# Performance work log

Measured on AMD Instinct MI355X. Metric: run time of the kernel, lower is better.

## Reference

```python
import jax, jax.numpy as jnp
import numpy as np

E = 1024   # embedding_dim
H = 16     # num_head
D = 64     # dim_head (E == H*D)
R = 8      # LoRA rank
BATCH = 2
SEQ = 2048
EPS = 1e-6


def setup_inputs() -> dict:
    key = jax.random.key(0)
    ks = jax.random.split(key, 16)
    s = 0.02
    return {
        "y": jax.random.normal(ks[0], (BATCH, SEQ, E), jnp.float32),
        "Wqkv": jax.random.normal(ks[1], (3 * E, E), jnp.float32) * s,
        "bqkv": jax.random.normal(ks[2], (3 * E,), jnp.float32) * s,
        "Wmsa": jax.random.normal(ks[3], (E, E), jnp.float32) * s,
        "Bq": jax.random.normal(ks[4], (E, R), jnp.float32) * s,
        "Aq": jax.random.normal(ks[5], (R, E), jnp.float32) * s,
        "Bk": jax.random.normal(ks[6], (E, R), jnp.float32) * s,
        "Ak": jax.random.normal(ks[7], (R, E), jnp.float32) * s,
        "Bv": jax.random.normal(ks[8], (E, R), jnp.float32) * s,
        "Av": jax.random.normal(ks[9], (R, E), jnp.float32) * s,
        "Bo": jax.random.normal(ks[10], (E, R), jnp.float32) * s,
        "Ao": jax.random.normal(ks[11], (R, E), jnp.float32) * s,
        "gamma": jnp.ones((E,), jnp.float32),
        "beta": jnp.zeros((E,), jnp.float32),
        "i": 0,
    }


def reference(y, Wqkv, bqkv, Wmsa, Bq, Aq, Bk, Ak, Bv, Av, Bo, Ao, gamma, beta, i):
    B, S, En = y.shape
    # fused QKV projection: nn.Linear -> y @ W.T + b
    qkv = (y @ Wqkv.T + bqkv).reshape(B, S, 3, H, D).transpose(2, 0, 3, 1, 4)
    Q, K, V = qkv[0], qkv[1], qkv[2]          # each [B,H,S,D]

    def lora_delta(Bw, Aw):
        # torch: y @ (B.weight @ A.weight), reshaped to heads
        return (y @ (Bw @ Aw)).reshape(B, S, H, D).transpose(0, 2, 1, 3)

    Q = Q + lora_delta(Bq, Aq)
    K = K + lora_delta(Bk, Ak)
    V = V + lora_delta(Bv, Av)

    scale = jnp.asarray(np.sqrt(D), y.dtype)
    scores = jnp.einsum('bhqd,bhkd->bhqk', Q, K) / scale
    attn = jax.nn.softmax(scores, axis=-1)
    o = jnp.einsum('bhqk,bhkd->bhqd', attn, V)          # [B,H,S,D]
    o = o.transpose(0, 2, 1, 3).reshape(B, S, H * D)    # [B,S,E]

    msa = o @ Wmsa.T + o @ (Bo @ Ao)
    res = msa + y

    mu = jnp.mean(res, axis=-1, keepdims=True)
    var = jnp.var(res, axis=-1, keepdims=True)
    return (res - mu) * jax.lax.rsqrt(var + EPS) * gamma + beta
```

## Files before the change

kernel.cpp:

```cpp
#include <hip/hip_runtime.h>
#include <hip/hip_bf16.h>
#include <stdint.h>

typedef __attribute__((ext_vector_type(8))) short short8;
typedef __attribute__((ext_vector_type(4))) float f32x4;

typedef const __attribute__((address_space(1))) void gv_t;
typedef __attribute__((address_space(3))) void lv_t;

#define SCQ 0.18033688011112042f

__device__ __forceinline__ void gl_lds16(const void* g, void* l) {
    __builtin_amdgcn_global_load_lds((gv_t*)g, (lv_t*)l, 16, 0, 0);
}

__device__ __forceinline__ unsigned short f2bf(float f) {
    union { float f; unsigned int u; } v; v.f = f;
    unsigned int r = v.u + 0x7fffu + ((v.u >> 16) & 1u);
    return (unsigned short)(r >> 16);
}

__device__ __forceinline__ unsigned int pack2bf(float a, float b) {
    union { __hip_bfloat162 h2; unsigned int u; } cv;
    cv.h2 = __float22bfloat162_rn(make_float2(a, b));
    return cv.u;
}

__device__ __forceinline__ f32x4 zero4() { f32x4 z = {0.f, 0.f, 0.f, 0.f}; return z; }

__global__ void k_cvt(const float* __restrict__ y, unsigned short* __restrict__ yb) {
    int i = (blockIdx.x * 256 + threadIdx.x) * 4;
    float4 v = *(const float4*)(y + i);
    union { unsigned short u[4]; uint2 w; } o;
    o.u[0] = f2bf(v.x); o.u[1] = f2bf(v.y); o.u[2] = f2bf(v.z); o.u[3] = f2bf(v.w);
    *(uint2*)(yb + i) = o.w;
}

__global__ void k_wqkv(const float* __restrict__ W,
                       const float* __restrict__ Bq, const float* __restrict__ Aq,
                       const float* __restrict__ Bk, const float* __restrict__ Ak,
                       const float* __restrict__ Bv, const float* __restrict__ Av,
                       unsigned short* __restrict__ out) {
    int idx = blockIdx.x * 256 + threadIdx.x;
    int n = idx >> 10, k = idx & 1023;
    int sel = n >> 10, n0 = n & 1023;
    const float* Bp = (sel == 0) ? Bq : (sel == 1) ? Bk : Bv;
    const float* Ap = (sel == 0) ? Aq : (sel == 1) ? Ak : Av;
    float acc = W[idx];
    #pragma unroll
    for (int r = 0; r < 8; ++r) acc += Bp[k * 8 + r] * Ap[r * 1024 + n0];
    out[idx] = f2bf(acc * ((sel == 0) ? SCQ : 1.0f));
}

__global__ void k_wmsa(const float* __restrict__ W,
                       const float* __restrict__ Bo, const float* __restrict__ Ao,
                       unsigned short* __restrict__ out) {
    int idx = blockIdx.x * 256 + threadIdx.x;
    int n = idx >> 10, k = idx & 1023;
    float acc = W[idx];
    #pragma unroll
    for (int r = 0; r < 8; ++r) acc += Bo[k * 8 + r] * Ao[r * 1024 + n];
    out[idx] = f2bf(acc);
}

template <int TM, int EPI>
__global__ __launch_bounds__(256, 2) void k_gemm(const unsigned short* __restrict__ Ag,
                                                 const unsigned short* __restrict__ Bg,
                                                 const float* __restrict__ bias,
                                                 const float* __restrict__ yres,
                                                 void* __restrict__ Cout,
                                                 int M, int N, int K) {
    constexpr int WAVES_N = 256 / TM;
    constexpr int WN = TM / 2;
    constexpr int NI = WN / 16;
    constexpr int ACALLS = TM / 64;
    __shared__ unsigned short As[2][TM * 32];
    __shared__ unsigned short Bs[2][128 * 32];
    const int flat = threadIdx.x;
    const int m0 = blockIdx.y * TM, n0 = blockIdx.x * 128;
    const int lane = flat & 63, wave = flat >> 6;
    const int l16 = lane & 15, quad = lane >> 4;
    const int wm = (wave / WAVES_N) * 64, wn = (wave % WAVES_N) * WN;

    f32x4 acc[4][NI];
    #pragma unroll
    for (int mi = 0; mi < 4; ++mi)
        #pragma unroll
        for (int ni = 0; ni < NI; ++ni) acc[mi][ni] = zero4();

    const unsigned short* ap = Ag + (size_t)(m0 + (flat >> 2)) * K + (flat & 3) * 8;
    const unsigned short* bp = Bg + (size_t)(n0 + (flat >> 2)) * K + (flat & 3) * 8;
    const size_t rstep = (size_t)64 * K;

    #pragma unroll
    for (int c = 0; c < ACALLS; ++c) gl_lds16(ap + c * rstep, &As[0][c * 2048 + flat * 8]);
    gl_lds16(bp,         &Bs[0][flat * 8]);
    gl_lds16(bp + rstep, &Bs[0][2048 + flat * 8]);
    ap += 32; bp += 32;
    __syncthreads();

    for (int k0 = 0; k0 < K; k0 += 32) {
        const int cur = (k0 >> 5) & 1;
        if (k0 + 32 < K) {
            const int nxt = cur ^ 1;
            #pragma unroll
            for (int c = 0; c < ACALLS; ++c) gl_lds16(ap + c * rstep, &As[nxt][c * 2048 + flat * 8]);
            gl_lds16(bp,         &Bs[nxt][flat * 8]);
            gl_lds16(bp + rstep, &Bs[nxt][2048 + flat * 8]);
            ap += 32; bp += 32;
        }

        short8 af[4], bfr[NI];
        #pragma unroll
        for (int i = 0; i < 4; ++i) af[i] = *(const short8*)&As[cur][(wm + i * 16 + l16) * 32 + quad * 8];
        #pragma unroll
        for (int i = 0; i < NI; ++i) bfr[i] = *(const short8*)&Bs[cur][(wn + i * 16 + l16) * 32 + quad * 8];
        #pragma unroll
        for (int mi = 0; mi < 4; ++mi)
            #pragma unroll
            for (int ni = 0; ni < NI; ++ni)
                acc[mi][ni] = __builtin_amdgcn_mfma_f32_16x16x32_bf16(af[mi], bfr[ni], acc[mi][ni], 0, 0, 0);

        __syncthreads();
    }

    if (EPI == 0) {
        unsigned short* C = (unsigned short*)Cout;
        #pragma unroll
        for (int ni = 0; ni < NI; ++ni) {
            int col = n0 + wn + ni * 16 + l16;
            float bv = bias[col] * ((col < 1024) ? SCQ : 1.0f);
            #pragma unroll
            for (int mi = 0; mi < 4; ++mi) {
                int row = m0 + wm + mi * 16 + quad * 4;
                #pragma unroll
                for (int r = 0; r < 4; ++r)
                    C[(size_t)(row + r) * N + col] = f2bf(acc[mi][ni][r] + bv);
            }
        }
    } else {
        float* C = (float*)Cout;
        #pragma unroll
        for (int ni = 0; ni < NI; ++ni) {
            int col = n0 + wn + ni * 16 + l16;
            #pragma unroll
            for (int mi = 0; mi < 4; ++mi) {
                int row = m0 + wm + mi * 16 + quad * 4;
                #pragma unroll
                for (int r = 0; r < 4; ++r)
                    C[(size_t)(row + r) * N + col] = acc[mi][ni][r] + yres[(size_t)(row + r) * N + col];
            }
        }
    }
}

__global__ __launch_bounds__(256) void k_vt(const unsigned short* __restrict__ qkv,
                                            unsigned short* __restrict__ vtg) {
    __shared__ unsigned short T[64 * 72];
    const int t = threadIdx.x;
    const int k0 = blockIdx.x * 64, h = blockIdx.y, b = blockIdx.z;
    const unsigned short* vbase = qkv + (size_t)(b * 2048) * 3072 + 2048 + h * 64;
    #pragma unroll
    for (int i = 0; i < 2; ++i) {
        int B = i * 256 + t;
        int row = B >> 3, c = B & 7;
        short8 v = *(const short8*)(vbase + (size_t)(k0 + row) * 3072 + c * 8);
        *(short8*)&T[row * 72 + c * 8] = v;
    }
    __syncthreads();
    unsigned short* obase = vtg + ((size_t)((b * 16 + h) * 64)) * 2048 + k0;
    #pragma unroll
    for (int i = 0; i < 2; ++i) {
        int B = i * 256 + t;
        int d = B >> 3, kc = B & 7;
        union { unsigned short u[8]; short8 v; } pk;
        #pragma unroll
        for (int jj = 0; jj < 8; ++jj) pk.u[jj] = T[(kc * 8 + jj) * 72 + d];
        *(short8*)(obase + (size_t)d * 2048 + kc * 8) = pk.v;
    }
}

__global__ __launch_bounds__(256, 2) void k_attn(const unsigned short* __restrict__ qkv,
                                                 const unsigned short* __restrict__ vtg,
                                                 unsigned short* __restrict__ o) {
    __shared__ unsigned short LDS[24576];
    unsigned short* Qs = LDS;
    unsigned short* Ps = LDS;
    unsigned short* Ks0 = LDS + 8192;
    unsigned short* Vt0 = LDS + 16384;

    const int t = threadIdx.x;
    const int lane = t & 63, wave = t >> 6;
    const int l16 = lane & 15, quad = lane >> 4;
    const int l8 = l16 & 7;
    const int q0 = blockIdx.x * 128;
    const int h = blockIdx.y, b = blockIdx.z;

    const unsigned short* qbase = qkv + (size_t)(b * 2048) * 3072 + h * 64;
    const unsigned short* kbase = qbase + 1024;
    const unsigned short* vtbase = vtg + (size_t)((b * 16 + h) * 64) * 2048;

    #pragma unroll
    for (int i = 0; i < 4; ++i) {
        int B = i * 256 + t;
        int row = B >> 3, c = (B & 7) ^ (row & 7);
        gl_lds16(qbase + (size_t)(q0 + row) * 3072 + c * 8, &Qs[B * 8]);
    }

    const int B0 = t, B1 = t + 256;
    const int r0 = B0 >> 3, c0 = (B0 & 7) ^ (r0 & 7);
    const int r1 = B1 >> 3, c1 = (B1 & 7) ^ (r1 & 7);
    const unsigned short* kp0 = kbase + (size_t)r0 * 3072 + c0 * 8;
    const unsigned short* kp1 = kbase + (size_t)r1 * 3072 + c1 * 8;
    const unsigned short* vp0 = vtbase + (size_t)r0 * 2048 + c0 * 8;
    const unsigned short* vp1 = vtbase + (size_t)r1 * 2048 + c1 * 8;

    gl_lds16(kp0, &Ks0[B0 * 8]);
    gl_lds16(kp1, &Ks0[B1 * 8]);
    gl_lds16(vp0, &Vt0[B0 * 8]);
    gl_lds16(vp1, &Vt0[B1 * 8]);
    kp0 += 64 * 3072; kp1 += 64 * 3072; vp0 += 64; vp1 += 64;

    __syncthreads();

    short8 qf[2][2];
    #pragma unroll
    for (int ni = 0; ni < 2; ++ni)
        #pragma unroll
        for (int kk = 0; kk < 2; ++kk)
            qf[ni][kk] = *(const short8*)&Qs[(wave * 32 + ni * 16 + l16) * 64 + ((kk * 4 + quad) ^ l8) * 8];

    __syncthreads();

    f32x4 acc_o[2][4];
    #pragma unroll
    for (int mo = 0; mo < 2; ++mo)
        #pragma unroll
        for (int nd = 0; nd < 4; ++nd) acc_o[mo][nd] = zero4();
    float lsum[2] = {0.f, 0.f};

    for (int j = 0; j < 32; ++j) {
        const unsigned short* Ks = Ks0 + (j & 1) * 4096;
        const unsigned short* Vt = Vt0 + (j & 1) * 4096;

        if (j < 31) {
            unsigned short* Kn = Ks0 + ((j + 1) & 1) * 4096;
            unsigned short* Vn = Vt0 + ((j + 1) & 1) * 4096;
            gl_lds16(kp0, &Kn[B0 * 8]);
            gl_lds16(kp1, &Kn[B1 * 8]);
            gl_lds16(vp0, &Vn[B0 * 8]);
            gl_lds16(vp1, &Vn[B1 * 8]);
            kp0 += 64 * 3072; kp1 += 64 * 3072; vp0 += 64; vp1 += 64;
        }

        f32x4 sacc[4][2];
        #pragma unroll
        for (int mi = 0; mi < 4; ++mi)
            #pragma unroll
            for (int ni = 0; ni < 2; ++ni) sacc[mi][ni] = zero4();
        #pragma unroll
        for (int kk = 0; kk < 2; ++kk)
            #pragma unroll
            for (int mi = 0; mi < 4; ++mi) {
                short8 kf = *(const short8*)&Ks[(mi * 16 + l16) * 64 + ((kk * 4 + quad) ^ l8) * 8];
                #pragma unroll
                for (int ni = 0; ni < 2; ++ni)
                    sacc[mi][ni] = __builtin_amdgcn_mfma_f32_16x16x32_bf16(kf, qf[ni][kk], sacc[mi][ni], 0, 0, 0);
            }

        #pragma unroll
        for (int ni = 0; ni < 2; ++ni) {
            int qrow = wave * 32 + ni * 16 + l16;
            #pragma unroll
            for (int mi = 0; mi < 4; ++mi) {
                float p0 = exp2f(sacc[mi][ni][0]);
                float p1 = exp2f(sacc[mi][ni][1]);
                float p2 = exp2f(sacc[mi][ni][2]);
                float p3 = exp2f(sacc[mi][ni][3]);
                lsum[ni] += (p0 + p1) + (p2 + p3);
                uint2 w; w.x = pack2bf(p0, p1); w.y = pack2bf(p2, p3);
                *(uint2*)&Ps[qrow * 64 + ((2 * mi + (quad >> 1)) ^ l8) * 8 + (quad & 1) * 4] = w;
            }
        }

        #pragma unroll
        for (int kk = 0; kk < 2; ++kk) {
            short8 pf[2];
            #pragma unroll
            for (int mo = 0; mo < 2; ++mo)
                pf[mo] = *(const short8*)&Ps[(wave * 32 + mo * 16 + l16) * 64 + ((kk * 4 + quad) ^ l8) * 8];
            #pragma unroll
            for (int nd = 0; nd < 4; ++nd) {
                short8 vf = *(const short8*)&Vt[(nd * 16 + l16) * 64 + ((kk * 4 + quad) ^ l8) * 8];
                #pragma unroll
                for (int mo = 0; mo < 2; ++mo)
                    acc_o[mo][nd] = __builtin_amdgcn_mfma_f32_16x16x32_bf16(pf[mo], vf, acc_o[mo][nd], 0, 0, 0);
            }
        }

        __syncthreads();
    }

    #pragma unroll
    for (int ni = 0; ni < 2; ++ni) {
        lsum[ni] += __shfl_xor(lsum[ni], 16);
        lsum[ni] += __shfl_xor(lsum[ni], 32);
    }
    #pragma unroll
    for (int mo = 0; mo < 2; ++mo)
        #pragma unroll
        for (int rr = 0; rr < 4; ++rr) {
            float lr = __shfl(lsum[mo], quad * 4 + rr, 16);
            float inv = 1.f / lr;
            int qg = q0 + wave * 32 + mo * 16 + quad * 4 + rr;
            size_t base = ((size_t)(b * 2048 + qg)) * 1024 + h * 64;
            #pragma unroll
            for (int nd = 0; nd < 4; ++nd)
                o[base + nd * 16 + l16] = f2bf(acc_o[mo][nd][rr] * inv);
        }
}

__global__ __launch_bounds__(256) void k_ln(const float* __restrict__ res,
                                            const float* __restrict__ g,
                                            const float* __restrict__ be,
                                            float* __restrict__ out) {
    __shared__ float red[8];
    const int row = blockIdx.x, t = threadIdx.x;
    const float* x = res + (size_t)row * 1024;
    float4 v = *(const float4*)(x + t * 4);
    float s = v.x + v.y + v.z + v.w;
    float sq = v.x * v.x + v.y * v.y + v.z * v.z + v.w * v.w;
    #pragma unroll
    for (int off = 32; off; off >>= 1) { s += __shfl_down(s, off); sq += __shfl_down(sq, off); }
    if ((t & 63) == 0) { red[t >> 6] = s; red[4 + (t >> 6)] = sq; }
    __syncthreads();
    float ts = red[0] + red[1] + red[2] + red[3];
    float tq = red[4] + red[5] + red[6] + red[7];
    float mu = ts * (1.f / 1024.f);
    float var = tq * (1.f / 1024.f) - mu * mu;
    float rstd = rsqrtf(var + 1e-6f);
    float4 gg = *(const float4*)(g + t * 4);
    float4 bb = *(const float4*)(be + t * 4);
    float4 ov;
    ov.x = (v.x - mu) * rstd * gg.x + bb.x;
    ov.y = (v.y - mu) * rstd * gg.y + bb.y;
    ov.z = (v.z - mu) * rstd * gg.z + bb.z;
    ov.w = (v.w - mu) * rstd * gg.w + bb.w;
    *(float4*)(out + (size_t)row * 1024 + t * 4) = ov;
}

extern "C" void kernel_launch(void* const* d_in, const int* in_sizes, int n_in,
                              void* d_out, int out_size, void* d_ws, size_t ws_size,
                              hipStream_t stream) {
    (void)in_sizes; (void)n_in; (void)out_size; (void)ws_size;
    const float* y    = (const float*)d_in[0];
    const float* Wqkv = (const float*)d_in[1];
    const float* bqkv = (const float*)d_in[2];
    const float* Wmsa = (const float*)d_in[3];
    const float* Bq = (const float*)d_in[4];
    const float* Aq = (const float*)d_in[5];
    const float* Bk = (const float*)d_in[6];
    const float* Ak = (const float*)d_in[7];
    const float* Bv = (const float*)d_in[8];
    const float* Av = (const float*)d_in[9];
    const float* Bo = (const float*)d_in[10];
    const float* Ao = (const float*)d_in[11];
    const float* gamma = (const float*)d_in[12];
    const float* beta  = (const float*)d_in[13];

    char* ws = (char*)d_ws;
    unsigned short* yb   = (unsigned short*)(ws);
    unsigned short* weq  = (unsigned short*)(ws + (8u  << 20));
    unsigned short* wem  = (unsigned short*)(ws + (14u << 20));
    unsigned short* qkv  = (unsigned short*)(ws + (16u << 20));
    unsigned short* vtg  = (unsigned short*)(ws + (40u << 20));
    unsigned short* obuf = yb;
    float* res = (float*)qkv;

    k_cvt <<<4096, 256, 0, stream>>>(y, yb);
    k_wqkv<<<12288, 256, 0, stream>>>(Wqkv, Bq, Aq, Bk, Ak, Bv, Av, weq);
    k_wmsa<<<4096, 256, 0, stream>>>(Wmsa, Bo, Ao, wem);
    k_gemm<128, 0><<<dim3(24, 32), 256, 0, stream>>>(yb, weq, bqkv, nullptr, (void*)qkv, 4096, 3072, 1024);
    k_vt  <<<dim3(32, 16, 2), 256, 0, stream>>>(qkv, vtg);
    k_attn<<<dim3(16, 16, 2), 256, 0, stream>>>(qkv, vtg, obuf);
    k_gemm<64, 1><<<dim3(8, 64), 256, 0, stream>>>(obuf, wem, nullptr, y, (void*)res, 4096, 1024, 1024);
    k_ln  <<<4096, 256, 0, stream>>>(res, gamma, beta, (float*)d_out);
}
```

Before: 241.0 us.

## Merge prep kernels, halve attention query tile, compute row sums via MFMA

Three preprocessing kernels (y conversion, QKV weight merge, MSA weight merge) become one launch that writes both merged weights into one contiguous buffer. The attention kernel drops from 128 to 64 query rows per block, doubling the grid and raising the occupancy hint to 4 blocks per CU. It also computes softmax denominators with an MFMA against a ones vector instead of scalar adds and shuffles, and uses the fast exp2/rcp builtins. GEMM launch-bound occupancy hints become template parameters (3 and 4). The trade-off is more K/V reloads per query and a possible register squeeze from the tighter launch bounds.

```diff
diff --git a/kernel.cpp b/kernel.cpp
--- a/kernel.cpp
+++ b/kernel.cpp
@@ -28,48 +28,40 @@
 
 __device__ __forceinline__ f32x4 zero4() { f32x4 z = {0.f, 0.f, 0.f, 0.f}; return z; }
 
-__global__ void k_cvt(const float* __restrict__ y, unsigned short* __restrict__ yb) {
-    int i = (blockIdx.x * 256 + threadIdx.x) * 4;
-    float4 v = *(const float4*)(y + i);
-    union { unsigned short u[4]; uint2 w; } o;
-    o.u[0] = f2bf(v.x); o.u[1] = f2bf(v.y); o.u[2] = f2bf(v.z); o.u[3] = f2bf(v.w);
-    *(uint2*)(yb + i) = o.w;
-}
-
-__global__ void k_wqkv(const float* __restrict__ W,
+__global__ void k_prep(const float* __restrict__ y,
+                       const float* __restrict__ Wqkv, const float* __restrict__ Wmsa,
                        const float* __restrict__ Bq, const float* __restrict__ Aq,
                        const float* __restrict__ Bk, const float* __restrict__ Ak,
                        const float* __restrict__ Bv, const float* __restrict__ Av,
-                       unsigned short* __restrict__ out) {
-    int idx = blockIdx.x * 256 + threadIdx.x;
-    int n = idx >> 10, k = idx & 1023;
-    int sel = n >> 10, n0 = n & 1023;
-    const float* Bp = (sel == 0) ? Bq : (sel == 1) ? Bk : Bv;
-    const float* Ap = (sel == 0) ? Aq : (sel == 1) ? Ak : Av;
-    float acc = W[idx];
-    #pragma unroll
-    for (int r = 0; r < 8; ++r) acc += Bp[k * 8 + r] * Ap[r * 1024 + n0];
-    out[idx] = f2bf(acc * ((sel == 0) ? SCQ : 1.0f));
-}
-
-__global__ void k_wmsa(const float* __restrict__ W,
                        const float* __restrict__ Bo, const float* __restrict__ Ao,
-                       unsigned short* __restrict__ out) {
-    int idx = blockIdx.x * 256 + threadIdx.x;
-    int n = idx >> 10, k = idx & 1023;
-    float acc = W[idx];
-    #pragma unroll
-    for (int r = 0; r < 8; ++r) acc += Bo[k * 8 + r] * Ao[r * 1024 + n];
-    out[idx] = f2bf(acc);
-}
-
-template <int TM, int EPI>
-__global__ __launch_bounds__(256, 2) void k_gemm(const unsigned short* __restrict__ Ag,
-                                                 const unsigned short* __restrict__ Bg,
-                                                 const float* __restrict__ bias,
-                                                 const float* __restrict__ yres,
-                                                 void* __restrict__ Cout,
-                                                 int M, int N, int K) {
+                       unsigned short* __restrict__ wout, unsigned short* __restrict__ yb) {
+    const int bid = blockIdx.x;
+    if (bid < 16384) {
+        int idx = bid * 256 + threadIdx.x;
+        int n = idx >> 10, k = idx & 1023;
+        int sel = n >> 10, n0 = n & 1023;
+        const float* Bp = (sel == 0) ? Bq : (sel == 1) ? Bk : (sel == 2) ? Bv : Bo;
+        const float* Ap = (sel == 0) ? Aq : (sel == 1) ? Ak : (sel == 2) ? Av : Ao;
+        float acc = (sel < 3) ? Wqkv[idx] : Wmsa[idx - 3145728];
+        #pragma unroll
+        for (int r = 0; r < 8; ++r) acc += Bp[k * 8 + r] * Ap[r * 1024 + n0];
+        wout[idx] = f2bf(acc * ((sel == 0) ? SCQ : 1.0f));
+    } else {
+        int i = ((bid - 16384) * 256 + threadIdx.x) * 4;
+        float4 v = *(const float4*)(y + i);
+        union { unsigned short u[4]; uint2 w; } o;
+        o.u[0] = f2bf(v.x); o.u[1] = f2bf(v.y); o.u[2] = f2bf(v.z); o.u[3] = f2bf(v.w);
+        *(uint2*)(yb + i) = o.w;
+    }
+}
+
+template <int TM, int EPI, int MINW>
+__global__ __launch_bounds__(256, MINW) void k_gemm(const unsigned short* __restrict__ Ag,
+                                                    const unsigned short* __restrict__ Bg,
+                                                    const float* __restrict__ bias,
+                                                    const float* __restrict__ yres,
+                                                    void* __restrict__ Cout,
+                                                    int M, int N, int K) {
     constexpr int WAVES_N = 256 / TM;
     constexpr int WN = TM / 2;
     constexpr int NI = WN / 16;
@@ -180,20 +172,20 @@
     }
 }
 
-__global__ __launch_bounds__(256, 2) void k_attn(const unsigned short* __restrict__ qkv,
+__global__ __launch_bounds__(256, 4) void k_attn(const unsigned short* __restrict__ qkv,
                                                  const unsigned short* __restrict__ vtg,
                                                  unsigned short* __restrict__ o) {
-    __shared__ unsigned short LDS[24576];
+    __shared__ unsigned short LDS[20480];
     unsigned short* Qs = LDS;
     unsigned short* Ps = LDS;
-    unsigned short* Ks0 = LDS + 8192;
-    unsigned short* Vt0 = LDS + 16384;
+    unsigned short* Ks0 = LDS + 4096;
+    unsigned short* Vt0 = LDS + 12288;
 
     const int t = threadIdx.x;
     const int lane = t & 63, wave = t >> 6;
     const int l16 = lane & 15, quad = lane >> 4;
     const int l8 = l16 & 7;
-    const int q0 = blockIdx.x * 128;
+    const int q0 = blockIdx.x * 64;
     const int h = blockIdx.y, b = blockIdx.z;
 
     const unsigned short* qbase = qkv + (size_t)(b * 2048) * 3072 + h * 64;
@@ -201,7 +193,7 @@
     const unsigned short* vtbase = vtg + (size_t)((b * 16 + h) * 64) * 2048;
 
     #pragma unroll
-    for (int i = 0; i < 4; ++i) {
+    for (int i = 0; i < 2; ++i) {
         int B = i * 256 + t;
         int row = B >> 3, c = (B & 7) ^ (row & 7);
         gl_lds16(qbase + (size_t)(q0 + row) * 3072 + c * 8, &Qs[B * 8]);
@@ -223,21 +215,20 @@
 
     __syncthreads();
 
-    short8 qf[2][2];
-    #pragma unroll
-    for (int ni = 0; ni < 2; ++ni)
-        #pragma unroll
-        for (int kk = 0; kk < 2; ++kk)
-            qf[ni][kk] = *(const short8*)&Qs[(wave * 32 + ni * 16 + l16) * 64 + ((kk * 4 + quad) ^ l8) * 8];
-
-    __syncthreads();
-
-    f32x4 acc_o[2][4];
-    #pragma unroll
-    for (int mo = 0; mo < 2; ++mo)
-        #pragma unroll
-        for (int nd = 0; nd < 4; ++nd) acc_o[mo][nd] = zero4();
-    float lsum[2] = {0.f, 0.f};
+    short8 qf[2];
+    #pragma unroll
+    for (int kk = 0; kk < 2; ++kk)
+        qf[kk] = *(const short8*)&Qs[(wave * 16 + l16) * 64 + ((kk * 4 + quad) ^ l8) * 8];
+
+    __syncthreads();
+
+    f32x4 acc_o[4];
+    #pragma unroll
+    for (int nd = 0; nd < 4; ++nd) acc_o[nd] = zero4();
+    f32x4 acc_l = zero4();
+    short8 ones;
+    #pragma unroll
+    for (int i = 0; i < 8; ++i) ones[i] = (short)0x3F80;
 
     for (int j = 0; j < 32; ++j) {
         const unsigned short* Ks = Ks0 + (j & 1) * 4096;
@@ -253,31 +244,25 @@
             kp0 += 64 * 3072; kp1 += 64 * 3072; vp0 += 64; vp1 += 64;
         }
 
-        f32x4 sacc[4][2];
-        #pragma unroll
-        for (int mi = 0; mi < 4; ++mi)
-            #pragma unroll
-            for (int ni = 0; ni < 2; ++ni) sacc[mi][ni] = zero4();
+        f32x4 sacc[4];
+        #pragma unroll
+        for (int mi = 0; mi < 4; ++mi) sacc[mi] = zero4();
         #pragma unroll
         for (int kk = 0; kk < 2; ++kk)
             #pragma unroll
             for (int mi = 0; mi < 4; ++mi) {
                 short8 kf = *(const short8*)&Ks[(mi * 16 + l16) * 64 + ((kk * 4 + quad) ^ l8) * 8];
-                #pragma unroll
-                for (int ni = 0; ni < 2; ++ni)
-                    sacc[mi][ni] = __builtin_amdgcn_mfma_f32_16x16x32_bf16(kf, qf[ni][kk], sacc[mi][ni], 0, 0, 0);
-            }
-
-        #pragma unroll
-        for (int ni = 0; ni < 2; ++ni) {
-            int qrow = wave * 32 + ni * 16 + l16;
+                sacc[mi] = __builtin_amdgcn_mfma_f32_16x16x32_bf16(kf, qf[kk], sacc[mi], 0, 0, 0);
+            }
+
+        {
+            int qrow = wave * 16 + l16;
             #pragma unroll
             for (int mi = 0; mi < 4; ++mi) {
-                float p0 = exp2f(sacc[mi][ni][0]);
-                float p1 = exp2f(sacc[mi][ni][1]);
-                float p2 = exp2f(sacc[mi][ni][2]);
-                float p3 = exp2f(sacc[mi][ni][3]);
-                lsum[ni] += (p0 + p1) + (p2 + p3);
+                float p0 = __builtin_amdgcn_exp2f(sacc[mi][0]);
+                float p1 = __builtin_amdgcn_exp2f(sacc[mi][1]);
+                float p2 = __builtin_amdgcn_exp2f(sacc[mi][2]);
+                float p3 = __builtin_amdgcn_exp2f(sacc[mi][3]);
                 uint2 w; w.x = pack2bf(p0, p1); w.y = pack2bf(p2, p3);
                 *(uint2*)&Ps[qrow * 64 + ((2 * mi + (quad >> 1)) ^ l8) * 8 + (quad & 1) * 4] = w;
             }
@@ -285,16 +270,12 @@
 
         #pragma unroll
         for (int kk = 0; kk < 2; ++kk) {
-            short8 pf[2];
-            #pragma unroll
-            for (int mo = 0; mo < 2; ++mo)
-                pf[mo] = *(const short8*)&Ps[(wave * 32 + mo * 16 + l16) * 64 + ((kk * 4 + quad) ^ l8) * 8];
+            short8 pf = *(const short8*)&Ps[(wave * 16 + l16) * 64 + ((kk * 4 + quad) ^ l8) * 8];
+            acc_l = __builtin_amdgcn_mfma_f32_16x16x32_bf16(pf, ones, acc_l, 0, 0, 0);
             #pragma unroll
             for (int nd = 0; nd < 4; ++nd) {
                 short8 vf = *(const short8*)&Vt[(nd * 16 + l16) * 64 + ((kk * 4 + quad) ^ l8) * 8];
-                #pragma unroll
-                for (int mo = 0; mo < 2; ++mo)
-                    acc_o[mo][nd] = __builtin_amdgcn_mfma_f32_16x16x32_bf16(pf[mo], vf, acc_o[mo][nd], 0, 0, 0);
+                acc_o[nd] = __builtin_amdgcn_mfma_f32_16x16x32_bf16(pf, vf, acc_o[nd], 0, 0, 0);
             }
         }
 
@@ -302,22 +283,14 @@
     }
 
     #pragma unroll
-    for (int ni = 0; ni < 2; ++ni) {
-        lsum[ni] += __shfl_xor(lsum[ni], 16);
-        lsum[ni] += __shfl_xor(lsum[ni], 32);
-    }
-    #pragma unroll
-    for (int mo = 0; mo < 2; ++mo)
-        #pragma unroll
-        for (int rr = 0; rr < 4; ++rr) {
-            float lr = __shfl(lsum[mo], quad * 4 + rr, 16);
-            float inv = 1.f / lr;
-            int qg = q0 + wave * 32 + mo * 16 + quad * 4 + rr;
-            size_t base = ((size_t)(b * 2048 + qg)) * 1024 + h * 64;
-            #pragma unroll
-            for (int nd = 0; nd < 4; ++nd)
-                o[base + nd * 16 + l16] = f2bf(acc_o[mo][nd][rr] * inv);
-        }
+    for (int rr = 0; rr < 4; ++rr) {
+        float inv = __builtin_amdgcn_rcpf(acc_l[rr]);
+        int qg = q0 + wave * 16 + quad * 4 + rr;
+        size_t base = ((size_t)(b * 2048 + qg)) * 1024 + h * 64;
+        #pragma unroll
+        for (int nd = 0; nd < 4; ++nd)
+            o[base + nd * 16 + l16] = f2bf(acc_o[nd][rr] * inv);
+    }
 }
 
 __global__ __launch_bounds__(256) void k_ln(const float* __restrict__ res,
@@ -371,18 +344,16 @@
     char* ws = (char*)d_ws;
     unsigned short* yb   = (unsigned short*)(ws);
     unsigned short* weq  = (unsigned short*)(ws + (8u  << 20));
-    unsigned short* wem  = (unsigned short*)(ws + (14u << 20));
     unsigned short* qkv  = (unsigned short*)(ws + (16u << 20));
     unsigned short* vtg  = (unsigned short*)(ws + (40u << 20));
+    unsigned short* wem  = weq + 3145728;
     unsigned short* obuf = yb;
     float* res = (float*)qkv;
 
-    k_cvt <<<4096, 256, 0, stream>>>(y, yb);
-    k_wqkv<<<12288, 256, 0, stream>>>(Wqkv, Bq, Aq, Bk, Ak, Bv, Av, weq);
-    k_wmsa<<<4096, 256, 0, stream>>>(Wmsa, Bo, Ao, wem);
-    k_gemm<128, 0><<<dim3(24, 32), 256, 0, stream>>>(yb, weq, bqkv, nullptr, (void*)qkv, 4096, 3072, 1024);
+    k_prep<<<17408, 256, 0, stream>>>(y, Wqkv, Wmsa, Bq, Aq, Bk, Ak, Bv, Av, Bo, Ao, weq, yb);
+    k_gemm<128, 0, 3><<<dim3(24, 32), 256, 0, stream>>>(yb, weq, bqkv, nullptr, (void*)qkv, 4096, 3072, 1024);
     k_vt  <<<dim3(32, 16, 2), 256, 0, stream>>>(qkv, vtg);
-    k_attn<<<dim3(16, 16, 2), 256, 0, stream>>>(qkv, vtg, obuf);
-    k_gemm<64, 1><<<dim3(8, 64), 256, 0, stream>>>(obuf, wem, nullptr, y, (void*)res, 4096, 1024, 1024);
+    k_attn<<<dim3(32, 16, 2), 256, 0, stream>>>(qkv, vtg, obuf);
+    k_gemm<64, 1, 4><<<dim3(8, 64), 256, 0, stream>>>(obuf, wem, nullptr, y, (void*)res, 4096, 1024, 1024);
     k_ln  <<<4096, 256, 0, stream>>>(res, gamma, beta, (float*)d_out);
 }
```

After: 220.7 us. 8.4% less time.

## Fuse prep kernels, write V transposed from QKV GEMM, MFMA row sums

Applied to the files above, without the earlier changes.

Merges the bf16 conversion of y and both LoRA-merged weight builds into one prep kernel. The QKV GEMM epilogue now writes the V columns directly in transposed layout, which removes the separate transpose kernel. In attention, softmax row sums are computed with an extra MFMA against a ones vector instead of scalar adds and shuffles, and exp2 uses the hardware builtin. Launch-bound occupancy hints are also raised, which may constrain register allocation and cause spills.

```diff
diff --git a/kernel.cpp b/kernel.cpp
--- a/kernel.cpp
+++ b/kernel.cpp
@@ -28,48 +28,41 @@
 
 __device__ __forceinline__ f32x4 zero4() { f32x4 z = {0.f, 0.f, 0.f, 0.f}; return z; }
 
-__global__ void k_cvt(const float* __restrict__ y, unsigned short* __restrict__ yb) {
-    int i = (blockIdx.x * 256 + threadIdx.x) * 4;
-    float4 v = *(const float4*)(y + i);
-    union { unsigned short u[4]; uint2 w; } o;
-    o.u[0] = f2bf(v.x); o.u[1] = f2bf(v.y); o.u[2] = f2bf(v.z); o.u[3] = f2bf(v.w);
-    *(uint2*)(yb + i) = o.w;
-}
-
-__global__ void k_wqkv(const float* __restrict__ W,
+__global__ void k_prep(const float* __restrict__ y,
+                       const float* __restrict__ Wqkv, const float* __restrict__ Wmsa,
                        const float* __restrict__ Bq, const float* __restrict__ Aq,
                        const float* __restrict__ Bk, const float* __restrict__ Ak,
                        const float* __restrict__ Bv, const float* __restrict__ Av,
-                       unsigned short* __restrict__ out) {
-    int idx = blockIdx.x * 256 + threadIdx.x;
-    int n = idx >> 10, k = idx & 1023;
-    int sel = n >> 10, n0 = n & 1023;
-    const float* Bp = (sel == 0) ? Bq : (sel == 1) ? Bk : Bv;
-    const float* Ap = (sel == 0) ? Aq : (sel == 1) ? Ak : Av;
-    float acc = W[idx];
-    #pragma unroll
-    for (int r = 0; r < 8; ++r) acc += Bp[k * 8 + r] * Ap[r * 1024 + n0];
-    out[idx] = f2bf(acc * ((sel == 0) ? SCQ : 1.0f));
-}
-
-__global__ void k_wmsa(const float* __restrict__ W,
                        const float* __restrict__ Bo, const float* __restrict__ Ao,
-                       unsigned short* __restrict__ out) {
-    int idx = blockIdx.x * 256 + threadIdx.x;
-    int n = idx >> 10, k = idx & 1023;
-    float acc = W[idx];
-    #pragma unroll
-    for (int r = 0; r < 8; ++r) acc += Bo[k * 8 + r] * Ao[r * 1024 + n];
-    out[idx] = f2bf(acc);
-}
-
-template <int TM, int EPI>
-__global__ __launch_bounds__(256, 2) void k_gemm(const unsigned short* __restrict__ Ag,
-                                                 const unsigned short* __restrict__ Bg,
-                                                 const float* __restrict__ bias,
-                                                 const float* __restrict__ yres,
-                                                 void* __restrict__ Cout,
-                                                 int M, int N, int K) {
+                       unsigned short* __restrict__ wout, unsigned short* __restrict__ yb) {
+    const int bid = blockIdx.x;
+    if (bid < 16384) {
+        int idx = bid * 256 + threadIdx.x;
+        int n = idx >> 10, k = idx & 1023;
+        int sel = n >> 10, n0 = n & 1023;
+        const float* Bp = (sel == 0) ? Bq : (sel == 1) ? Bk : (sel == 2) ? Bv : Bo;
+        const float* Ap = (sel == 0) ? Aq : (sel == 1) ? Ak : (sel == 2) ? Av : Ao;
+        float acc = (sel < 3) ? Wqkv[idx] : Wmsa[idx - 3145728];
+        #pragma unroll
+        for (int r = 0; r < 8; ++r) acc += Bp[k * 8 + r] * Ap[r * 1024 + n0];
+        wout[idx] = f2bf(acc * ((sel == 0) ? SCQ : 1.0f));
+    } else {
+        int i = ((bid - 16384) * 256 + threadIdx.x) * 4;
+        float4 v = *(const float4*)(y + i);
+        union { unsigned short u[4]; uint2 w; } o;
+        o.u[0] = f2bf(v.x); o.u[1] = f2bf(v.y); o.u[2] = f2bf(v.z); o.u[3] = f2bf(v.w);
+        *(uint2*)(yb + i) = o.w;
+    }
+}
+
+template <int TM, int EPI, int MINW>
+__global__ __launch_bounds__(256, MINW) void k_gemm(const unsigned short* __restrict__ Ag,
+                                                    const unsigned short* __restrict__ Bg,
+                                                    const float* __restrict__ bias,
+                                                    const float* __restrict__ yres,
+                                                    unsigned short* __restrict__ vtg,
+                                                    void* __restrict__ Cout,
+                                                    int M, int N, int K) {
     constexpr int WAVES_N = 256 / TM;
     constexpr int WN = TM / 2;
     constexpr int NI = WN / 16;
@@ -126,61 +119,54 @@
 
     if (EPI == 0) {
         unsigned short* C = (unsigned short*)Cout;
+        if (n0 < 2048) {
+            #pragma unroll
+            for (int ni = 0; ni < NI; ++ni) {
+                int col = n0 + wn + ni * 16 + l16;
+                float bv = bias[col] * ((col < 1024) ? SCQ : 1.0f);
+                #pragma unroll
+                for (int mi = 0; mi < 4; ++mi) {
+                    int row = m0 + wm + mi * 16 + quad * 4;
+                    #pragma unroll
+                    for (int r = 0; r < 4; ++r)
+                        C[(size_t)(row + r) * N + col] = f2bf(acc[mi][ni][r] + bv);
+                }
+            }
+        } else {
+            #pragma unroll
+            for (int ni = 0; ni < NI; ++ni) {
+                int col = n0 + wn + ni * 16 + l16;
+                float bv = bias[col];
+                int hh = (col - 2048) >> 6, dd = col & 63;
+                unsigned short* vrow0 = vtg + (size_t)(hh * 64 + dd) * 2048;
+                #pragma unroll
+                for (int mi = 0; mi < 4; ++mi) {
+                    int row = m0 + wm + mi * 16 + quad * 4;
+                    int bb = row >> 11, ss = row & 2047;
+                    uint2 w;
+                    w.x = pack2bf(acc[mi][ni][0] + bv, acc[mi][ni][1] + bv);
+                    w.y = pack2bf(acc[mi][ni][2] + bv, acc[mi][ni][3] + bv);
+                    *(uint2*)(vrow0 + (size_t)bb * 2097152 + ss) = w;
+                }
+            }
+        }
+    } else {
+        float* C = (float*)Cout;
         #pragma unroll
         for (int ni = 0; ni < NI; ++ni) {
             int col = n0 + wn + ni * 16 + l16;
-            float bv = bias[col] * ((col < 1024) ? SCQ : 1.0f);
             #pragma unroll
             for (int mi = 0; mi < 4; ++mi) {
                 int row = m0 + wm + mi * 16 + quad * 4;
                 #pragma unroll
                 for (int r = 0; r < 4; ++r)
-                    C[(size_t)(row + r) * N + col] = f2bf(acc[mi][ni][r] + bv);
-            }
-        }
-    } else {
-        float* C = (float*)Cout;
-        #pragma unroll
-        for (int ni = 0; ni < NI; ++ni) {
-            int col = n0 + wn + ni * 16 + l16;
-            #pragma unroll
-            for (int mi = 0; mi < 4; ++mi) {
-                int row = m0 + wm + mi * 16 + quad * 4;
-                #pragma unroll
-                for (int r = 0; r < 4; ++r)
                     C[(size_t)(row + r) * N + col] = acc[mi][ni][r] + yres[(size_t)(row + r) * N + col];
             }
         }
     }
 }
 
-__global__ __launch_bounds__(256) void k_vt(const unsigned short* __restrict__ qkv,
-                                            unsigned short* __restrict__ vtg) {
-    __shared__ unsigned short T[64 * 72];
-    const int t = threadIdx.x;
-    const int k0 = blockIdx.x * 64, h = blockIdx.y, b = blockIdx.z;
-    const unsigned short* vbase = qkv + (size_t)(b * 2048) * 3072 + 2048 + h * 64;
-    #pragma unroll
-    for (int i = 0; i < 2; ++i) {
-        int B = i * 256 + t;
-        int row = B >> 3, c = B & 7;
-        short8 v = *(const short8*)(vbase + (size_t)(k0 + row) * 3072 + c * 8);
-        *(short8*)&T[row * 72 + c * 8] = v;
-    }
-    __syncthreads();
-    unsigned short* obase = vtg + ((size_t)((b * 16 + h) * 64)) * 2048 + k0;
-    #pragma unroll
-    for (int i = 0; i < 2; ++i) {
-        int B = i * 256 + t;
-        int d = B >> 3, kc = B & 7;
-        union { unsigned short u[8]; short8 v; } pk;
-        #pragma unroll
-        for (int jj = 0; jj < 8; ++jj) pk.u[jj] = T[(kc * 8 + jj) * 72 + d];
-        *(short8*)(obase + (size_t)d * 2048 + kc * 8) = pk.v;
-    }
-}
-
-__global__ __launch_bounds__(256, 2) void k_attn(const unsigned short* __restrict__ qkv,
+__global__ __launch_bounds__(256, 3) void k_attn(const unsigned short* __restrict__ qkv,
                                                  const unsigned short* __restrict__ vtg,
                                                  unsigned short* __restrict__ o) {
     __shared__ unsigned short LDS[24576];
@@ -237,7 +223,10 @@
     for (int mo = 0; mo < 2; ++mo)
         #pragma unroll
         for (int nd = 0; nd < 4; ++nd) acc_o[mo][nd] = zero4();
-    float lsum[2] = {0.f, 0.f};
+    f32x4 acc_l[2] = {zero4(), zero4()};
+    short8 ones;
+    #pragma unroll
+    for (int i = 0; i < 8; ++i) ones[i] = (short)0x3F80;
 
     for (int j = 0; j < 32; ++j) {
         const unsigned short* Ks = Ks0 + (j & 1) * 4096;
@@ -273,11 +262,10 @@
             int qrow = wave * 32 + ni * 16 + l16;
             #pragma unroll
             for (int mi = 0; mi < 4; ++mi) {
-                float p0 = exp2f(sacc[mi][ni][0]);
-                float p1 = exp2f(sacc[mi][ni][1]);
-                float p2 = exp2f(sacc[mi][ni][2]);
-                float p3 = exp2f(sacc[mi][ni][3]);
-                lsum[ni] += (p0 + p1) + (p2 + p3);
+                float p0 = __builtin_amdgcn_exp2f(sacc[mi][ni][0]);
+                float p1 = __builtin_amdgcn_exp2f(sacc[mi][ni][1]);
+                float p2 = __builtin_amdgcn_exp2f(sacc[mi][ni][2]);
+                float p3 = __builtin_amdgcn_exp2f(sacc[mi][ni][3]);
                 uint2 w; w.x = pack2bf(p0, p1); w.y = pack2bf(p2, p3);
                 *(uint2*)&Ps[qrow * 64 + ((2 * mi + (quad >> 1)) ^ l8) * 8 + (quad & 1) * 4] = w;
             }
@@ -287,8 +275,10 @@
         for (int kk = 0; kk < 2; ++kk) {
             short8 pf[2];
             #pragma unroll
-            for (int mo = 0; mo < 2; ++mo)
+            for (int mo = 0; mo < 2; ++mo) {
                 pf[mo] = *(const short8*)&Ps[(wave * 32 + mo * 16 + l16) * 64 + ((kk * 4 + quad) ^ l8) * 8];
+                acc_l[mo] = __builtin_amdgcn_mfma_f32_16x16x32_bf16(pf[mo], ones, acc_l[mo], 0, 0, 0);
+            }
             #pragma unroll
             for (int nd = 0; nd < 4; ++nd) {
                 short8 vf = *(const short8*)&Vt[(nd * 16 + l16) * 64 + ((kk * 4 + quad) ^ l8) * 8];
@@ -302,16 +292,10 @@
     }
 
     #pragma unroll
-    for (int ni = 0; ni < 2; ++ni) {
-        lsum[ni] += __shfl_xor(lsum[ni], 16);
-        lsum[ni] += __shfl_xor(lsum[ni], 32);
-    }
-    #pragma unroll
     for (int mo = 0; mo < 2; ++mo)
         #pragma unroll
         for (int rr = 0; rr < 4; ++rr) {
-            float lr = __shfl(lsum[mo], quad * 4 + rr, 16);
-            float inv = 1.f / lr;
+            float inv = 1.0f / acc_l[mo][rr];
             int qg = q0 + wave * 32 + mo * 16 + quad * 4 + rr;
             size_t base = ((size_t)(b * 2048 + qg)) * 1024 + h * 64;
             #pragma unroll
@@ -371,18 +355,15 @@
     char* ws = (char*)d_ws;
     unsigned short* yb   = (unsigned short*)(ws);
     unsigned short* weq  = (unsigned short*)(ws + (8u  << 20));
-    unsigned short* wem  = (unsigned short*)(ws + (14u << 20));
     unsigned short* qkv  = (unsigned short*)(ws + (16u << 20));
     unsigned short* vtg  = (unsigned short*)(ws + (40u << 20));
+    unsigned short* wem  = weq + 3145728;
     unsigned short* obuf = yb;
     float* res = (float*)qkv;
 
-    k_cvt <<<4096, 256, 0, stream>>>(y, yb);
-    k_wqkv<<<12288, 256, 0, stream>>>(Wqkv, Bq, Aq, Bk, Ak, Bv, Av, weq);
-    k_wmsa<<<4096, 256, 0, stream>>>(Wmsa, Bo, Ao, wem);
-    k_gemm<128, 0><<<dim3(24, 32), 256, 0, stream>>>(yb, weq, bqkv, nullptr, (void*)qkv, 4096, 3072, 1024);
-    k_vt  <<<dim3(32, 16, 2), 256, 0, stream>>>(qkv, vtg);
+    k_prep<<<17408, 256, 0, stream>>>(y, Wqkv, Wmsa, Bq, Aq, Bk, Ak, Bv, Av, Bo, Ao, weq, yb);
+    k_gemm<128, 0, 3><<<dim3(24, 32), 256, 0, stream>>>(yb, weq, bqkv, nullptr, vtg, (void*)qkv, 4096, 3072, 1024);
     k_attn<<<dim3(16, 16, 2), 256, 0, stream>>>(qkv, vtg, obuf);
-    k_gemm<64, 1><<<dim3(8, 64), 256, 0, stream>>>(obuf, wem, nullptr, y, (void*)res, 4096, 1024, 1024);
+    k_gemm<64, 1, 4><<<dim3(8, 64), 256, 0, stream>>>(obuf, wem, nullptr, y, nullptr, (void*)res, 4096, 1024, 1024);
     k_ln  <<<4096, 256, 0, stream>>>(res, gamma, beta, (float*)d_out);
 }
```

Result: faster. 214.3 us (-11.1%).
